# Optimization experiments

Hardware: AMD Instinct MI355X
Metric: run time of the kernel (lower is better)

The kernel has to match this reference:

```python
import jax, jax.numpy as jnp
import numpy as np

BN_EPS = 1e-5
SLOPE = 0.01  # LeakyReLU negative slope (torch default)


def setup_inputs() -> dict:
    key = jax.random.key(0)
    ks = jax.random.split(key, 16)
    N, E = 100000, 1600000
    Cin, C, S, L, Lc = 64, 128, 256, 3, 2
    inp = {}
    inp["x"] = jax.random.normal(ks[0], (N, Cin), jnp.float32)
    inp["edge_index"] = jax.random.randint(ks[1], (2, E), 0, N, jnp.int32)
    inp["batch"] = jnp.zeros((N,), jnp.int32)
    # first GIN layer params
    inp["eps1"] = jnp.zeros((1,), jnp.float32)
    inp["W1"] = jax.random.normal(ks[2], (Cin, C), jnp.float32) * (1.0 / np.sqrt(Cin))
    inp["b1"] = jnp.zeros((C,), jnp.float32)
    inp["g1"] = jnp.ones((C,), jnp.float32)
    inp["be1"] = jnp.zeros((C,), jnp.float32)
    inp["m1"] = jnp.zeros((C,), jnp.float32)
    inp["v1"] = jax.random.uniform(ks[3], (C,), jnp.float32, 0.5, 1.5)
    # stacked GIN layers
    inp["epsL"] = jnp.zeros((L,), jnp.float32)
    inp["WL"] = jax.random.normal(ks[4], (L, C, C), jnp.float32) * (1.0 / np.sqrt(C))
    inp["bL"] = jnp.zeros((L, C), jnp.float32)
    inp["gL"] = jnp.ones((L, C), jnp.float32)
    inp["beL"] = jnp.zeros((L, C), jnp.float32)
    inp["mL"] = jnp.zeros((L, C), jnp.float32)
    inp["vL"] = jax.random.uniform(ks[5], (L, C), jnp.float32, 0.5, 1.5)
    # classifier
    inp["Wc1"] = jax.random.normal(ks[6], (C, S), jnp.float32) * (1.0 / np.sqrt(C))
    inp["bc1"] = jnp.zeros((S,), jnp.float32)
    inp["Wcl"] = jax.random.normal(ks[7], (Lc, S, S), jnp.float32) * (1.0 / np.sqrt(S))
    inp["bcl"] = jnp.zeros((Lc, S), jnp.float32)
    inp["Wf"] = jax.random.normal(ks[8], (S, 1), jnp.float32) * (1.0 / np.sqrt(S))
    inp["bf"] = jnp.zeros((1,), jnp.float32)
    return inp


def reference(x, edge_index, batch, eps1, W1, b1, g1, be1, m1, v1,
              epsL, WL, bL, gL, beL, mL, vL, Wc1, bc1, Wcl, bcl, Wf, bf):
    N = x.shape[0]
    src, dst = edge_index[0], edge_index[1]
    lrelu = lambda z: jnp.where(z >= 0, z, SLOPE * z)

    def gin(h, eps, W, b, g, be, m, v):
        # scatter-add neighbor aggregation: aggr[i] = sum_{(j->i) in E} h[j]
        aggr = jax.ops.segment_sum(h[src], dst, num_segments=N)
        z = ((1.0 + eps) * h + aggr) @ W + b          # Linear
        z = (z - m) * (g * jax.lax.rsqrt(v + BN_EPS)) + be  # BatchNorm (inference)
        return lrelu(z)                                # LeakyReLU in MLP; Dropout=identity

    h = lrelu(gin(x, eps1, W1, b1, g1, be1, m1, v1))  # outer leaky_relu in forward
    for i in range(WL.shape[0]):
        h = lrelu(gin(h, epsL[i], WL[i], bL[i], gL[i], beL[i], mL[i], vL[i]))
    h = h @ Wc1 + bc1
    for i in range(Wcl.shape[0]):
        h = lrelu(h @ Wcl[i] + bcl[i])
    return jax.nn.sigmoid(h @ Wf + bf)  # [N, 1]
```

## Files before the change

### kernel.cpp

```cpp
#include <hip/hip_runtime.h>
#include <stdint.h>


#define NN  100000
#define EE  1600000
#define CIN 64
#define CC  128
#define NBK 782
#define CHUNK 8192
#define NCH 196

typedef __attribute__((ext_vector_type(8))) __bf16 bf16x8;
typedef __attribute__((ext_vector_type(4))) float  f32x4;

__device__ __forceinline__ float bf2f(uint32_t u) { return __uint_as_float(u << 16); }
__device__ __forceinline__ float bf2f_hi(uint32_t u) { return __uint_as_float(u & 0xffff0000u); }
__device__ __forceinline__ ushort f2bf(float f) {
  uint32_t u = __float_as_uint(f);
  u += 0x7fffu + ((u >> 16) & 1u);
  return (ushort)(u >> 16);
}

template<int ACT> __device__ __forceinline__ float actf(float z) {
  if constexpr (ACT == 1) return z >= 0.f ? z : 0.01f * z;
  else if constexpr (ACT == 2) return z >= 0.f ? z : 1e-4f * z;
  else return z;
}

__device__ __forceinline__ void gload_lds16(const void* g, void* l) {
  __builtin_amdgcn_global_load_lds(
      (const __attribute__((address_space(1))) void*)g,
      (__attribute__((address_space(3))) void*)l, 16, 0, 0);
}

__global__ __launch_bounds__(256) void ms_hist_kernel(const int* __restrict__ ei,
                                                      int* __restrict__ hist,
                                                      int* __restrict__ bh, int e) {
  __shared__ int h[NBK];
  for (int i = threadIdx.x; i < NBK; i += 256) h[i] = 0;
  __syncthreads();
  const int base = blockIdx.x * CHUNK;
  const int end = min(base + CHUNK, e);
  for (int i = base + threadIdx.x; i < end; i += 256)
    atomicAdd(&h[ei[e + i] >> 7], 1);
  __syncthreads();
  for (int i = threadIdx.x; i < NBK; i += 256) {
    hist[blockIdx.x * NBK + i] = h[i];
    if (h[i]) atomicAdd(&bh[i], h[i]);
  }
}

__global__ __launch_bounds__(256) void bkt_scan_kernel(const int* __restrict__ bh,
                                                       int* __restrict__ boff, int e) {
  __shared__ int sd[256];
  int t = threadIdx.x;
  int base = t * 4;
  int v0 = base + 0 < NBK ? bh[base + 0] : 0;
  int v1 = base + 1 < NBK ? bh[base + 1] : 0;
  int v2 = base + 2 < NBK ? bh[base + 2] : 0;
  int v3 = base + 3 < NBK ? bh[base + 3] : 0;
  int ts = v0 + v1 + v2 + v3;
  sd[t] = ts; __syncthreads();
  for (int off = 1; off < 256; off <<= 1) {
    int u = (t >= off) ? sd[t - off] : 0;
    __syncthreads();
    sd[t] += u;
    __syncthreads();
  }
  int excl = sd[t] - ts;
  if (base + 0 < NBK) boff[base + 0] = excl;
  if (base + 1 < NBK) boff[base + 1] = excl + v0;
  if (base + 2 < NBK) boff[base + 2] = excl + v0 + v1;
  if (base + 3 < NBK) boff[base + 3] = excl + v0 + v1 + v2;
  if (t == 255) boff[NBK] = e;
}

__global__ void ms_offs_kernel(int* __restrict__ hist, const int* __restrict__ boff) {
  int b = blockIdx.x * 256 + threadIdx.x;
  if (b >= NBK) return;
  int run = boff[b];
  for (int k = 0; k < NCH; ++k) {
    int t = hist[k * NBK + b];
    hist[k * NBK + b] = run;
    run += t;
  }
}

__global__ __launch_bounds__(256) void ms_scatter_kernel(const int* __restrict__ ei,
                                                         const int* __restrict__ hist,
                                                         uint* __restrict__ ebkt, int e) {
  __shared__ int cur[NBK];
  for (int i = threadIdx.x; i < NBK; i += 256) cur[i] = hist[blockIdx.x * NBK + i];
  __syncthreads();
  const int base = blockIdx.x * CHUNK;
  const int end = min(base + CHUNK, e);
  for (int i = base + threadIdx.x; i < end; i += 256) {
    int s = ei[i], d = ei[e + i];
    int p = atomicAdd(&cur[d >> 7], 1);
    ebkt[p] = ((uint)(d & 127) << 17) | (uint)s;
  }
}

__global__ __launch_bounds__(256) void bkt_deg_kernel(const uint* __restrict__ ebkt,
                                                      const int* __restrict__ boff,
                                                      int* __restrict__ deg, int n) {
  __shared__ int dl[128];
  int b = blockIdx.x;
  for (int i = threadIdx.x; i < 128; i += 256) dl[i] = 0;
  __syncthreads();
  int j1 = boff[b + 1];
  for (int j = boff[b] + threadIdx.x; j < j1; j += 256)
    atomicAdd(&dl[ebkt[j] >> 17], 1);
  __syncthreads();
  for (int i = threadIdx.x; i < 128; i += 256) {
    int node = (b << 7) + i;
    if (node < n) deg[node] = dl[i];
  }
}

__global__ __launch_bounds__(256) void bkt_fill_kernel(const uint* __restrict__ ebkt,
                                                       const int* __restrict__ boff,
                                                       const int* __restrict__ rowp,
                                                       int* __restrict__ colb, int n) {
  __shared__ int cur[128];
  int b = blockIdx.x;
  for (int i = threadIdx.x; i < 128; i += 256) {
    int node = (b << 7) + i;
    cur[i] = (node < n) ? rowp[node] : 0;
  }
  __syncthreads();
  int j1 = boff[b + 1];
  for (int j = boff[b] + threadIdx.x; j < j1; j += 256) {
    uint v = ebkt[j];
    int p = atomicAdd(&cur[v >> 17], 1);
    colb[p] = (int)(v & 0x1FFFFu);
  }
}

__global__ void scan1_kernel(const int* __restrict__ deg, int* __restrict__ outp,
                             int* __restrict__ partial, int n) {
  __shared__ int sd[256];
  int t = threadIdx.x;
  int base = blockIdx.x * 1024 + t * 4;
  int v0 = base + 0 < n ? deg[base + 0] : 0;
  int v1 = base + 1 < n ? deg[base + 1] : 0;
  int v2 = base + 2 < n ? deg[base + 2] : 0;
  int v3 = base + 3 < n ? deg[base + 3] : 0;
  int ts = v0 + v1 + v2 + v3;
  sd[t] = ts; __syncthreads();
  for (int off = 1; off < 256; off <<= 1) {
    int u = (t >= off) ? sd[t - off] : 0;
    __syncthreads();
    sd[t] += u;
    __syncthreads();
  }
  int excl = sd[t] - ts;
  if (base + 0 < n) outp[base + 0] = excl;
  if (base + 1 < n) outp[base + 1] = excl + v0;
  if (base + 2 < n) outp[base + 2] = excl + v0 + v1;
  if (base + 3 < n) outp[base + 3] = excl + v0 + v1 + v2;
  if (t == 255) partial[blockIdx.x] = sd[255];
}

__global__ void scan2_kernel(int* __restrict__ partial, int nb) {
  __shared__ int sd[256];
  int t = threadIdx.x;
  int v = t < nb ? partial[t] : 0;
  sd[t] = v; __syncthreads();
  for (int off = 1; off < 256; off <<= 1) {
    int u = (t >= off) ? sd[t - off] : 0;
    __syncthreads();
    sd[t] += u;
    __syncthreads();
  }
  if (t < nb) partial[t] = sd[t] - v;
}

__global__ void scan3_kernel(int* __restrict__ rowp, const int* __restrict__ partial,
                             int n, int e) {
  int i = blockIdx.x * 256 + threadIdx.x;
  if (i == 0) rowp[n] = e;
  if (i < n) rowp[i] += partial[i >> 10];
}

__global__ void bnprep_kernel(const float* b1, const float* g1, const float* be1,
                              const float* m1, const float* v1,
                              const float* bL, const float* gL, const float* beL,
                              const float* mL, const float* vL,
                              float* __restrict__ sc, float* __restrict__ tc) {
  int i = blockIdx.x * 256 + threadIdx.x;
  if (i >= 4 * 128) return;
  int layer = i >> 7, c = i & 127;
  float b, g, be, m, v;
  if (layer == 0) { b = b1[c]; g = g1[c]; be = be1[c]; m = m1[c]; v = v1[c]; }
  else { int o = (layer - 1) * 128 + c; b = bL[o]; g = gL[o]; be = beL[o]; m = mL[o]; v = vL[o]; }
  float s = g * rsqrtf(v + 1e-5f);
  sc[i] = s;
  tc[i] = (b - m) * s + be;
}

__global__ void wtprep_kernel(const float* __restrict__ W1, const float* __restrict__ WL,
                              const float* __restrict__ Wc1, const float* __restrict__ Wcl,
                              ushort* __restrict__ wt1, ushort* __restrict__ wtL,
                              ushort* __restrict__ wtc1, ushort* __restrict__ wtcl) {
  int i = blockIdx.x * 256 + threadIdx.x;
  if (i < 8192) {
    int m = i >> 6, k = i & 63;
    wt1[i] = f2bf(W1[k * 128 + m]);
  } else if (i < 8192 + 49152) {
    int j = i - 8192;
    int l = j >> 14, r = j & 16383, m = r >> 7, k = r & 127;
    wtL[j] = f2bf(WL[l * 16384 + k * 128 + m]);
  } else if (i < 8192 + 49152 + 32768) {
    int j = i - (8192 + 49152);
    int m = j >> 7, k = j & 127;
    wtc1[j] = f2bf(Wc1[k * 256 + m]);
  } else if (i < 8192 + 49152 + 32768 + 131072) {
    int j = i - (8192 + 49152 + 32768);
    int l = j >> 16, r = j & 65535, m = r >> 8, k = r & 255;
    wtcl[j] = f2bf(Wcl[l * 65536 + k * 256 + m]);
  }
}

__global__ void xconv_kernel(const float* __restrict__ x, ushort* __restrict__ xb, int n4) {
  int i = blockIdx.x * 256 + threadIdx.x;
  if (i < n4) {
    float4 v = ((const float4*)x)[i];
    ushort4 o;
    o.x = f2bf(v.x); o.y = f2bf(v.y); o.z = f2bf(v.z); o.w = f2bf(v.w);
    ((ushort4*)xb)[i] = o;
  }
}

template<int C>
__global__ __launch_bounds__(256) void agg_kernel(
    const ushort* __restrict__ hb, const int* __restrict__ rowp,
    const int* __restrict__ colb, const float* __restrict__ ep,
    ushort* __restrict__ zout, int n)
{
  constexpr int LPE = C / 8;
  constexpr int EPR = 64 / LPE;
  const int lane = threadIdx.x & 63;
  const int node = blockIdx.x * 4 + (threadIdx.x >> 6);
  if (node >= n) return;
  const float e1 = 1.0f + ep[0];
  const int lo = lane & (LPE - 1);
  const int g  = lane / LPE;
  int j0 = rowp[node], jend = rowp[node + 1];

  float a0 = 0.f, a1 = 0.f, a2 = 0.f, a3 = 0.f,
        a4 = 0.f, a5 = 0.f, a6 = 0.f, a7 = 0.f;

  for (; j0 < jend; j0 += 64) {
    int cnt = jend - j0; if (cnt > 64) cnt = 64;
    int myn = (lane < cnt) ? colb[j0 + lane] : 0;
    int rounds = (cnt + EPR - 1) / EPR;
    #pragma unroll 4
    for (int r = 0; r < rounds; ++r) {
      int e = r * EPR + g;
      int u = __shfl(myn, e);
      if (e < cnt) {
        const uint4 v = *(const uint4*)(hb + (size_t)u * C + lo * 8);
        a0 += bf2f(v.x); a1 += bf2f_hi(v.x);
        a2 += bf2f(v.y); a3 += bf2f_hi(v.y);
        a4 += bf2f(v.z); a5 += bf2f_hi(v.z);
        a6 += bf2f(v.w); a7 += bf2f_hi(v.w);
      }
    }
  }

  #pragma unroll
  for (int s = LPE; s < 64; s <<= 1) {
    a0 += __shfl_xor(a0, s); a1 += __shfl_xor(a1, s);
    a2 += __shfl_xor(a2, s); a3 += __shfl_xor(a3, s);
    a4 += __shfl_xor(a4, s); a5 += __shfl_xor(a5, s);
    a6 += __shfl_xor(a6, s); a7 += __shfl_xor(a7, s);
  }

  if (g == 0) {
    const uint4 d = *(const uint4*)(hb + (size_t)node * C + lo * 8);
    uint4 o;
    o.x = (uint)f2bf(e1 * bf2f(d.x) + a0) | ((uint)f2bf(e1 * bf2f_hi(d.x) + a1) << 16);
    o.y = (uint)f2bf(e1 * bf2f(d.y) + a2) | ((uint)f2bf(e1 * bf2f_hi(d.y) + a3) << 16);
    o.z = (uint)f2bf(e1 * bf2f(d.z) + a4) | ((uint)f2bf(e1 * bf2f_hi(d.z) + a5) << 16);
    o.w = (uint)f2bf(e1 * bf2f(d.w) + a6) | ((uint)f2bf(e1 * bf2f_hi(d.w) + a7) << 16);
    *(uint4*)(zout + (size_t)node * C + lo * 8) = o;
  }
}

template<int K, int M, int ACT, bool BN>
__global__ __launch_bounds__(256) void gemm_kernel(
    const ushort* __restrict__ xin,
    const ushort* __restrict__ wt,
    const float*  __restrict__ sc,
    const float*  __restrict__ tc,
    ushort* __restrict__ hout,
    int n)
{
  constexpr int KS = 64;
  __shared__ ushort ldsW[128 * KS];
  __shared__ ushort ldsX[128 * KS];
  const int tid = threadIdx.x;
  const int wave = tid >> 6, lane = tid & 63;
  const int lr = lane & 15, lg = lane >> 4;
  const int n0 = blockIdx.x * 128;
  const int mB = blockIdx.y * 128;

  f32x4 acc[8][2];
  #pragma unroll
  for (int r = 0; r < 8; ++r) {
    acc[r][0] = (f32x4){0.f, 0.f, 0.f, 0.f};
    acc[r][1] = (f32x4){0.f, 0.f, 0.f, 0.f};
  }

  #pragma unroll
  for (int s = 0; s < K / KS; ++s) {
    if (s) __syncthreads();
    #pragma unroll
    for (int i = 0; i < 4; ++i) {
      const int ub = wave * 4096 + i * 1024;
      const int a  = ub + lane * 16;
      const int m  = a >> 7;
      const int o  = (a & 127) ^ ((m & 7) << 4);
      gload_lds16((const char*)wt + ((size_t)(mB + m) * K) * 2 + s * 128 + o,
                  (char*)ldsW + ub);
      int nd = n0 + m; if (nd >= n) nd = n - 1;
      gload_lds16((const char*)xin + ((size_t)nd * K) * 2 + s * 128 + o,
                  (char*)ldsX + ub);
    }
    asm volatile("s_waitcnt vmcnt(0)" ::: "memory");
    __syncthreads();
    #pragma unroll
    for (int k0 = 0; k0 < KS; k0 += 32) {
      const int kb = (k0 + lg * 8) * 2;
      bf16x8 wf0, wf1;
      {
        int m = wave * 32 + lr;
        wf0 = __builtin_bit_cast(bf16x8,
              *(const uint4*)((const char*)ldsW + ((m * 128 + kb) ^ ((m & 7) << 4))));
        m += 16;
        wf1 = __builtin_bit_cast(bf16x8,
              *(const uint4*)((const char*)ldsW + ((m * 128 + kb) ^ ((m & 7) << 4))));
      }
      #pragma unroll
      for (int r = 0; r < 8; ++r) {
        int xr = r * 16 + lr;
        bf16x8 xf = __builtin_bit_cast(bf16x8,
              *(const uint4*)((const char*)ldsX + ((xr * 128 + kb) ^ ((xr & 7) << 4))));
        acc[r][0] = __builtin_amdgcn_mfma_f32_16x16x32_bf16(wf0, xf, acc[r][0], 0, 0, 0);
        acc[r][1] = __builtin_amdgcn_mfma_f32_16x16x32_bf16(wf1, xf, acc[r][1], 0, 0, 0);
      }
    }
  }

  #pragma unroll
  for (int ct = 0; ct < 2; ++ct) {
    const int c0 = mB + wave * 32 + ct * 16 + lg * 4;
    float4 sv;
    if constexpr (BN) sv = *(const float4*)(sc + c0);
    else sv = make_float4(1.f, 1.f, 1.f, 1.f);
    const float4 tv = *(const float4*)(tc + c0);
    #pragma unroll
    for (int r = 0; r < 8; ++r) {
      const int node = n0 + r * 16 + lr;
      if (node < n) {
        const f32x4 a = acc[r][ct];
        ushort4 o;
        o.x = f2bf(actf<ACT>(a[0] * sv.x + tv.x));
        o.y = f2bf(actf<ACT>(a[1] * sv.y + tv.y));
        o.z = f2bf(actf<ACT>(a[2] * sv.z + tv.z));
        o.w = f2bf(actf<ACT>(a[3] * sv.w + tv.w));
        *(ushort4*)(hout + (size_t)node * M + c0) = o;
      }
    }
  }
}

__global__ __launch_bounds__(256) void final_kernel(
    const ushort* __restrict__ s, const float* __restrict__ wf,
    const float* __restrict__ bfp, float* __restrict__ out, int n)
{
  const int lane = threadIdx.x & 63;
  const int node = blockIdx.x * 4 + (threadIdx.x >> 6);
  if (node >= n) return;
  const uint2 d = *(const uint2*)(s + (size_t)node * 256 + lane * 4);
  const float4 w = *(const float4*)(wf + lane * 4);
  float acc = bf2f(d.x & 0xffff) * w.x + bf2f(d.x >> 16) * w.y
            + bf2f(d.y & 0xffff) * w.z + bf2f(d.y >> 16) * w.w;
  for (int off = 32; off; off >>= 1) acc += __shfl_down(acc, off);
  if (lane == 0) out[node] = 1.f / (1.f + expf(-(acc + bfp[0])));
}

extern "C" void kernel_launch(void* const* d_in, const int* in_sizes, int n_in,
                              void* d_out, int out_size, void* d_ws, size_t ws_size,
                              hipStream_t stream)
{
  const float* x    = (const float*)d_in[0];
  const int*   ei   = (const int*)d_in[1];
  const float* eps1 = (const float*)d_in[3];
  const float* W1   = (const float*)d_in[4];
  const float* b1   = (const float*)d_in[5];
  const float* g1   = (const float*)d_in[6];
  const float* be1  = (const float*)d_in[7];
  const float* m1   = (const float*)d_in[8];
  const float* v1   = (const float*)d_in[9];
  const float* epsL = (const float*)d_in[10];
  const float* WL   = (const float*)d_in[11];
  const float* bL   = (const float*)d_in[12];
  const float* gL   = (const float*)d_in[13];
  const float* beL  = (const float*)d_in[14];
  const float* mL   = (const float*)d_in[15];
  const float* vL   = (const float*)d_in[16];
  const float* Wc1  = (const float*)d_in[17];
  const float* bc1  = (const float*)d_in[18];
  const float* Wcl  = (const float*)d_in[19];
  const float* bcl  = (const float*)d_in[20];
  const float* Wf   = (const float*)d_in[21];
  const float* bfp  = (const float*)d_in[22];
  float* out = (float*)d_out;

  char* w = (char*)d_ws;
  size_t off = 0;
  auto alloc = [&](size_t bytes) {
    char* p = w + off;
    off += (bytes + 255) & ~(size_t)255;
    return p;
  };
  ushort* bufA   = (ushort*)alloc((size_t)NN * 256 * 2);
  ushort* bufB   = (ushort*)alloc((size_t)NN * 256 * 2);
  int*    rowp   = (int*)alloc((NN + 1) * 4);
  int*    deg    = (int*)alloc(NN * 4);
  int*    colb   = (int*)alloc((size_t)EE * 4);
  uint*   ebkt   = (uint*)alloc((size_t)EE * 4);
  int*    hist   = (int*)alloc((size_t)NCH * NBK * 4);
  int*    bh     = (int*)alloc(NBK * 4);
  int*    boff   = (int*)alloc((NBK + 1) * 4);
  int*    partial= (int*)alloc(1024);
  ushort* wt1    = (ushort*)alloc(8192 * 2);
  ushort* wtL    = (ushort*)alloc(49152 * 2);
  ushort* wtc1   = (ushort*)alloc(32768 * 2);
  ushort* wtcl   = (ushort*)alloc(131072 * 2);
  float*  sc     = (float*)alloc(512 * 4);
  float*  tc     = (float*)alloc(512 * 4);
  (void)ws_size; (void)in_sizes; (void)n_in; (void)out_size;

  hipMemsetAsync(bh, 0, NBK * 4, stream);
  ms_hist_kernel<<<NCH, 256, 0, stream>>>(ei, hist, bh, EE);
  bkt_scan_kernel<<<1, 256, 0, stream>>>(bh, boff, EE);
  ms_offs_kernel<<<(NBK + 255) / 256, 256, 0, stream>>>(hist, boff);
  ms_scatter_kernel<<<NCH, 256, 0, stream>>>(ei, hist, ebkt, EE);
  bkt_deg_kernel<<<NBK, 256, 0, stream>>>(ebkt, boff, deg, NN);
  scan1_kernel<<<98, 256, 0, stream>>>(deg, rowp, partial, NN);
  scan2_kernel<<<1, 256, 0, stream>>>(partial, 98);
  scan3_kernel<<<(NN + 255) / 256, 256, 0, stream>>>(rowp, partial, NN, EE);
  bkt_fill_kernel<<<NBK, 256, 0, stream>>>(ebkt, boff, rowp, colb, NN);

  bnprep_kernel<<<2, 256, 0, stream>>>(b1, g1, be1, m1, v1, bL, gL, beL, mL, vL, sc, tc);
  wtprep_kernel<<<864, 256, 0, stream>>>(W1, WL, Wc1, Wcl, wt1, wtL, wtc1, wtcl);
  xconv_kernel<<<(NN * CIN / 4 + 255) / 256, 256, 0, stream>>>(x, bufA, NN * CIN / 4);

  const int GB = (NN + 127) / 128;

  agg_kernel<64><<<25000, 256, 0, stream>>>(bufA, rowp, colb, eps1, bufB, NN);
  gemm_kernel<64, 128, 2, true><<<dim3(GB, 1), 256, 0, stream>>>(bufB, wt1, sc, tc, bufA, NN);
  for (int i = 0; i < 3; ++i) {
    agg_kernel<128><<<25000, 256, 0, stream>>>(bufA, rowp, colb, epsL + i, bufB, NN);
    gemm_kernel<128, 128, 2, true><<<dim3(GB, 1), 256, 0, stream>>>(
        bufB, wtL + i * 16384, sc + 128 * (i + 1), tc + 128 * (i + 1), bufA, NN);
  }
  gemm_kernel<128, 256, 0, false><<<dim3(GB, 2), 256, 0, stream>>>(bufA, wtc1, nullptr, bc1, bufB, NN);
  gemm_kernel<256, 256, 1, false><<<dim3(GB, 2), 256, 0, stream>>>(bufB, wtcl, nullptr, bcl, bufA, NN);
  gemm_kernel<256, 256, 1, false><<<dim3(GB, 2), 256, 0, stream>>>(bufA, wtcl + 65536, nullptr, bcl + 256, bufB, NN);
  final_kernel<<<25000, 256, 0, stream>>>(bufB, Wf, bfp, out, NN);
}
```

Measured before the change: 510.5 us.

## Fuse classifier MLP and final sigmoid into one LDS-resident kernel

Replaces three classifier GEMM launches and the final dot-product kernel with a single kernel. Each block keeps its 128-node by 256-wide hidden activations in shared memory across all three layers and streams weight slabs with double buffering. The last layer's output is reduced against Wf in registers before the sigmoid. This removes intermediate global writes and reads of 256-wide bf16 activations, but it needs 144KB of LDS per block, which limits occupancy to one block per CU and produces only about 782 blocks.

New measurement: 476.4 us. 1.07x faster.

```diff
diff --git a/kernel.cpp b/kernel.cpp
--- a/kernel.cpp
+++ b/kernel.cpp
@@ -376,19 +376,169 @@
   }
 }
 
-__global__ __launch_bounds__(256) void final_kernel(
-    const ushort* __restrict__ s, const float* __restrict__ wf,
-    const float* __restrict__ bfp, float* __restrict__ out, int n)
+__global__ __launch_bounds__(256) void cls_kernel(
+    const ushort* __restrict__ xin,
+    const ushort* __restrict__ wc1,
+    const float*  __restrict__ bc1,
+    const ushort* __restrict__ wcl,
+    const float*  __restrict__ bcl,
+    const float*  __restrict__ wfv,
+    const float*  __restrict__ bfp,
+    float* __restrict__ out, int n)
 {
-  const int lane = threadIdx.x & 63;
-  const int node = blockIdx.x * 4 + (threadIdx.x >> 6);
-  if (node >= n) return;
-  const uint2 d = *(const uint2*)(s + (size_t)node * 256 + lane * 4);
-  const float4 w = *(const float4*)(wf + lane * 4);
-  float acc = bf2f(d.x & 0xffff) * w.x + bf2f(d.x >> 16) * w.y
-            + bf2f(d.y & 0xffff) * w.z + bf2f(d.y >> 16) * w.w;
-  for (int off = 32; off; off >>= 1) acc += __shfl_down(acc, off);
-  if (lane == 0) out[node] = 1.f / (1.f + expf(-(acc + bfp[0])));
+  extern __shared__ char lds[];
+  char* ldsW0 = lds;
+  char* ldsW1 = lds + 32768;
+  char* ldsH  = lds + 65536;
+  char* ldsX  = lds + 131072;
+  const int tid = threadIdx.x;
+  const int wave = tid >> 6, lane = tid & 63;
+  const int lr = lane & 15, lg = lane >> 4;
+  const int n0 = blockIdx.x * 128;
+
+  f32x4 acc[8][4];
+
+  auto stageW = [&](const ushort* wsrc, int K2, int s, char* dst) {
+    #pragma unroll
+    for (int i = 0; i < 8; ++i) {
+      const int ub = wave * 8192 + i * 1024;
+      const int a = ub + lane * 16;
+      const int m = a >> 7;
+      const int o = (a & 127) ^ ((m & 7) << 4);
+      gload_lds16((const char*)wsrc + (size_t)m * K2 * 2 + s * 128 + o, dst + ub);
+    }
+  };
+  auto stageX = [&](int s) {
+    #pragma unroll
+    for (int i = 0; i < 4; ++i) {
+      const int ub = wave * 4096 + i * 1024;
+      const int a = ub + lane * 16;
+      const int m = a >> 7;
+      const int o = (a & 127) ^ ((m & 7) << 4);
+      int nd = n0 + m; if (nd >= n) nd = n - 1;
+      gload_lds16((const char*)xin + (size_t)nd * 128 * 2 + s * 128 + o, ldsX + ub);
+    }
+  };
+  auto mfma_slab = [&](const char* wbuf, const char* xbase, int rowOff) {
+    #pragma unroll
+    for (int k0 = 0; k0 < 64; k0 += 32) {
+      const int kb = (k0 + lg * 8) * 2;
+      bf16x8 wfr[4];
+      #pragma unroll
+      for (int ct = 0; ct < 4; ++ct) {
+        int m = wave * 64 + ct * 16 + lr;
+        wfr[ct] = __builtin_bit_cast(bf16x8,
+                  *(const uint4*)(wbuf + ((m * 128 + kb) ^ ((m & 7) << 4))));
+      }
+      #pragma unroll
+      for (int r = 0; r < 8; ++r) {
+        int xr = rowOff + r * 16 + lr;
+        bf16x8 xf = __builtin_bit_cast(bf16x8,
+                    *(const uint4*)(xbase + ((xr * 128 + kb) ^ ((xr & 7) << 4))));
+        #pragma unroll
+        for (int ct = 0; ct < 4; ++ct)
+          acc[r][ct] = __builtin_amdgcn_mfma_f32_16x16x32_bf16(wfr[ct], xf, acc[r][ct], 0, 0, 0);
+      }
+    }
+  };
+  auto zacc = [&]() {
+    #pragma unroll
+    for (int r = 0; r < 8; ++r)
+      #pragma unroll
+      for (int c = 0; c < 4; ++c) acc[r][c] = (f32x4){0.f, 0.f, 0.f, 0.f};
+  };
+
+  zacc();
+  #pragma unroll
+  for (int s = 0; s < 2; ++s) {
+    if (s) __syncthreads();
+    stageX(s);
+    stageW(wc1, 128, s, ldsW0);
+    asm volatile("s_waitcnt vmcnt(0)" ::: "memory");
+    __syncthreads();
+    mfma_slab(ldsW0, ldsX, 0);
+  }
+  __syncthreads();
+  #pragma unroll
+  for (int ct = 0; ct < 4; ++ct) {
+    const int c0 = wave * 64 + ct * 16 + lg * 4;
+    const float4 bv = *(const float4*)(bc1 + c0);
+    #pragma unroll
+    for (int r = 0; r < 8; ++r) {
+      const int nl = r * 16 + lr;
+      const int rowH = wave * 128 + nl;
+      const f32x4 a = acc[r][ct];
+      ushort4 o;
+      o.x = f2bf(a[0] + bv.x); o.y = f2bf(a[1] + bv.y);
+      o.z = f2bf(a[2] + bv.z); o.w = f2bf(a[3] + bv.w);
+      *(ushort4*)(ldsH + ((rowH * 128 + (c0 & 63) * 2) ^ ((rowH & 7) << 4))) = o;
+    }
+  }
+
+  for (int g = 0; g < 2; ++g) {
+    const ushort* Wg = wcl + g * 65536;
+    const float*  bg = bcl + g * 256;
+    zacc();
+    __syncthreads();
+    stageW(Wg, 256, 0, ldsW0);
+    #pragma unroll
+    for (int s = 0; s < 4; ++s) {
+      char* cur = (s & 1) ? ldsW1 : ldsW0;
+      char* nxt = (s & 1) ? ldsW0 : ldsW1;
+      if (s + 1 < 4) {
+        stageW(Wg, 256, s + 1, nxt);
+        asm volatile("s_waitcnt vmcnt(8)" ::: "memory");
+      } else {
+        asm volatile("s_waitcnt vmcnt(0)" ::: "memory");
+      }
+      __syncthreads();
+      mfma_slab(cur, ldsH, s * 128);
+      __syncthreads();
+    }
+    if (g == 0) {
+      #pragma unroll
+      for (int ct = 0; ct < 4; ++ct) {
+        const int c0 = wave * 64 + ct * 16 + lg * 4;
+        const float4 bv = *(const float4*)(bg + c0);
+        #pragma unroll
+        for (int r = 0; r < 8; ++r) {
+          const int nl = r * 16 + lr;
+          const int rowH = wave * 128 + nl;
+          const f32x4 a = acc[r][ct];
+          ushort4 o;
+          o.x = f2bf(actf<1>(a[0] + bv.x)); o.y = f2bf(actf<1>(a[1] + bv.y));
+          o.z = f2bf(actf<1>(a[2] + bv.z)); o.w = f2bf(actf<1>(a[3] + bv.w));
+          *(ushort4*)(ldsH + ((rowH * 128 + (c0 & 63) * 2) ^ ((rowH & 7) << 4))) = o;
+        }
+      }
+    } else {
+      float* red = (float*)ldsX;
+      #pragma unroll
+      for (int r = 0; r < 8; ++r) {
+        float p = 0.f;
+        #pragma unroll
+        for (int ct = 0; ct < 4; ++ct) {
+          const int c0 = wave * 64 + ct * 16 + lg * 4;
+          const float4 bv = *(const float4*)(bg + c0);
+          const float4 wv = *(const float4*)(wfv + c0);
+          const f32x4 a = acc[r][ct];
+          p += actf<1>(a[0] + bv.x) * wv.x + actf<1>(a[1] + bv.y) * wv.y
+             + actf<1>(a[2] + bv.z) * wv.z + actf<1>(a[3] + bv.w) * wv.w;
+        }
+        p += __shfl_xor(p, 16);
+        p += __shfl_xor(p, 32);
+        if (lg == 0) red[wave * 128 + r * 16 + lr] = p;
+      }
+      __syncthreads();
+      if (tid < 128) {
+        const int nd = n0 + tid;
+        if (nd < n) {
+          float logit = red[tid] + red[128 + tid] + red[256 + tid] + red[384 + tid] + bfp[0];
+          out[nd] = 1.f / (1.f + expf(-logit));
+        }
+      }
+    }
+  }
 }
 
 extern "C" void kernel_launch(void* const* d_in, const int* in_sizes, int n_in,
@@ -468,8 +618,7 @@
     gemm_kernel<128, 128, 2, true><<<dim3(GB, 1), 256, 0, stream>>>(
         bufB, wtL + i * 16384, sc + 128 * (i + 1), tc + 128 * (i + 1), bufA, NN);
   }
-  gemm_kernel<128, 256, 0, false><<<dim3(GB, 2), 256, 0, stream>>>(bufA, wtc1, nullptr, bc1, bufB, NN);
-  gemm_kernel<256, 256, 1, false><<<dim3(GB, 2), 256, 0, stream>>>(bufB, wtcl, nullptr, bcl, bufA, NN);
-  gemm_kernel<256, 256, 1, false><<<dim3(GB, 2), 256, 0, stream>>>(bufA, wtcl + 65536, nullptr, bcl + 256, bufB, NN);
-  final_kernel<<<25000, 256, 0, stream>>>(bufB, Wf, bfp, out, NN);
-}
+  hipFuncSetAttribute(reinterpret_cast<const void*>(cls_kernel),
+                      hipFuncAttributeMaxDynamicSharedMemorySize, 147456);
+  cls_kernel<<<GB, 256, 147456, stream>>>(bufA, wtc1, bc1, wtcl, bcl, Wf, bfp, out, NN);
+}
```
